# Kernel tuning notes

Measured on AMD Instinct MI355X. Metric: run time of the kernel, lower is better.

## Reference

```python
import jax, jax.numpy as jnp
import numpy as np

VOCAB, EMB, HID = 32000, 512, 1024
B, T = 16, 128


def setup_inputs() -> dict:
    key = jax.random.key(0)
    ks = jax.random.split(key, 12)
    bound = 1.0 / np.sqrt(HID)
    u = lambda k, shape: jax.random.uniform(k, shape, jnp.float32, -bound, bound)
    return {
        "sentence": jax.random.randint(ks[0], (B, T), 0, VOCAB),
        "emb": jax.random.normal(ks[1], (VOCAB, EMB), jnp.float32),
        "W_i": u(ks[2], (EMB + HID, HID)), "b_i": u(ks[3], (HID,)),
        "W_f": u(ks[4], (EMB + HID, HID)), "b_f": u(ks[5], (HID,)),
        "W_o": u(ks[6], (EMB + HID, HID)), "b_o": u(ks[7], (HID,)),
        "W_c": u(ks[8], (EMB + HID, HID)), "b_c": u(ks[9], (HID,)),
        "W_hq": u(ks[10], (HID, VOCAB)), "b_q": u(ks[11], (VOCAB,)),
    }


def reference(sentence, emb, W_i, b_i, W_f, b_f, W_o, b_o, W_c, b_c, W_hq, b_q):
    # [B,T,E] -> [T,B,E]
    x = jnp.swapaxes(emb[sentence], 0, 1)
    # Fuse the 4 gate matmuls into one concatenated-weight matmul (same math).
    W = jnp.concatenate([W_i, W_f, W_o, W_c], axis=1)  # [E+H, 4H]
    b = jnp.concatenate([b_i, b_f, b_o, b_c])          # [4H]
    h0 = jnp.zeros((x.shape[1], HID), x.dtype)

    def step(carry, xt):
        h, c = carry
        z = jnp.concatenate([xt, h], axis=1) @ W + b   # [B,4H]
        i, f, o, g = jnp.split(z, 4, axis=1)
        i, f, o = jax.nn.sigmoid(i), jax.nn.sigmoid(f), jax.nn.sigmoid(o)
        c = f * c + i * jnp.tanh(g)
        h = o * jnp.tanh(c)
        return (h, c), h

    _, hs = jax.lax.scan(step, (h0, h0), x)            # [T,B,H]
    out = jnp.einsum('tbh,hv->tbv', hs, W_hq) + b_q    # [T,B,V]
    return jnp.transpose(out, (1, 2, 0))               # [B,V,T] as in torch permute(1,2,0)
```

## Files before the change

kernel.cpp:

```cpp
#include <hip/hip_runtime.h>
#include <math.h>

typedef float f32x4 __attribute__((ext_vector_type(4)));
typedef short bf16x8 __attribute__((ext_vector_type(8)));
typedef unsigned short u16;
typedef unsigned int u32;
typedef unsigned long long u64;

#define FLAG_STRIDE 16
#define ACQ_BASE    8192
#define EPOCH_BASE  8448
#define QCNT_BASE   8512
#define TCNT_BASE   8528
#define FLAG_WORDS  ((TCNT_BASE + 1) * FLAG_STRIDE)
#define NTILE       125

__device__ __forceinline__ u16 f2bf(float f) {
    union { float f; unsigned u; } x; x.f = f;
    unsigned r = x.u + 0x7fff + ((x.u >> 16) & 1);
    return (u16)(r >> 16);
}

__device__ __forceinline__ void gload_lds16(const u16* g, u16* l) {
    __builtin_amdgcn_global_load_lds(
        (const __attribute__((address_space(1))) void*)g,
        (__attribute__((address_space(3))) void*)l, 16, 0, 0);
}

__global__ __launch_bounds__(256) void prep(
    const int* __restrict__ sent, const float* __restrict__ emb, u16* __restrict__ xb) {
    const int bx = blockIdx.x, tid = threadIdx.x;
    int row = bx * 2 + (tid >> 7);
    int t = row >> 4, b = row & 15;
    int idx = sent[b * 128 + t];
    float4 v = ((const float4*)(emb + (size_t)idx * 512))[tid & 127];
    ushort4 s = { f2bf(v.x), f2bf(v.y), f2bf(v.z), f2bf(v.w) };
    ((ushort4*)(xb + (size_t)row * 512))[tid & 127] = s;
}

__global__ __launch_bounds__(512, 2) void lstm_proj(
    u16* __restrict__ hs,
    const u16* __restrict__ xb,
    const float* __restrict__ Wi, const float* __restrict__ Wf,
    const float* __restrict__ Wo, const float* __restrict__ Wc,
    const float* __restrict__ bi, const float* __restrict__ bf_,
    const float* __restrict__ bo, const float* __restrict__ bc,
    u32* __restrict__ flags,
    const float* __restrict__ Whq,
    u16* __restrict__ whqt,
    const float* __restrict__ bq, float* __restrict__ out) {
    __shared__ __align__(16) char smem[135680];
    const int bx = blockIdx.x;
    const int tid = threadIdx.x;
    const int w = tid >> 6, l = tid & 63;

    if (tid == 0)
        __hip_atomic_fetch_add(&flags[(size_t)(ACQ_BASE + (bx & 255)) * FLAG_STRIDE], 0u,
                               __ATOMIC_ACQ_REL, __HIP_MEMORY_SCOPE_AGENT);

    if (bx < 64) {
        u16* hstage = (u16*)smem;
        u16* xstage = (u16*)(smem + 32768);
        u16* wfx    = (u16*)(smem + 65536);
        float (*zlds)[16][17] = (float (*)[16][17])(void*)(smem + 131072);
        u32* lds_cnt = (u32*)(smem + 135424);
        const int j = bx;
        const int row = l & 15, hi = l >> 4;
        if (tid == 0) *lds_cnt = 0;

        bf16x8 wf[32];
        if (w < 4) {
            const float* Wg = (w == 0) ? Wi : (w == 1) ? Wf : (w == 2) ? Wo : Wc;
#pragma unroll
            for (int kk = 0; kk < 32; ++kk)
#pragma unroll
                for (int e = 0; e < 8; ++e)
                    wf[kk][e] = f2bf(Wg[(size_t)(512 + kk * 32 + hi * 8 + e) * 1024 + j * 16 + row]);
#pragma unroll
            for (int kk = 0; kk < 16; ++kk) {
                bf16x8 v;
#pragma unroll
                for (int e = 0; e < 8; ++e)
                    v[e] = f2bf(Wg[(size_t)(kk * 32 + hi * 8 + e) * 1024 + j * 16 + row]);
                *(bf16x8*)(wfx + ((size_t)(w * 16 + kk) * 64 + l) * 8) = v;
            }
        }
        float bzi = 0.f, bzf = 0.f, bzo = 0.f, bzc = 0.f;
        const int b = tid >> 4, hc = tid & 15;
        if (tid < 256) {
            bzi = bi[j * 16 + hc]; bzf = bf_[j * 16 + hc];
            bzo = bo[j * 16 + hc]; bzc = bc[j * 16 + hc];
        }
#pragma unroll
        for (int q = 0; q < 2; ++q) {
            int jx0 = (w * 2 + q) * 2;
            gload_lds16(xb + (size_t)((l & 31) >> 1) * 512 + (jx0 + (l >> 5)) * 16 + (l & 1) * 8,
                        xstage + (size_t)jx0 * 256);
        }
        __syncthreads();

        float cst = 0.f;

        for (int t = 0; t < 128; ++t) {
            if (t < 127) {
                const u16* xbase = xb + (size_t)(t + 1) * 16 * 512;
                u16* xd = xstage + ((t + 1) & 1) * 8192;
#pragma unroll
                for (int q = 0; q < 2; ++q) {
                    int jx0 = (w * 2 + q) * 2;
                    gload_lds16(xbase + (size_t)((l & 31) >> 1) * 512 + (jx0 + (l >> 5)) * 16 + (l & 1) * 8,
                                xd + (size_t)jx0 * 256);
                }
            }
            if (t > 0) {
                const u16* hbase = hs + (size_t)(t - 1) * 16 * 1024;
                {
                    int spins = 0;
                    while (true) {
                        u32 f = 1u;
                        if (l < 8)
                            f = __hip_atomic_load(
                                    &flags[(size_t)((t - 1) * 64 + 8 * w + l) * FLAG_STRIDE],
                                    __ATOMIC_RELAXED, __HIP_MEMORY_SCOPE_SYSTEM);
                        if (__ballot(f != 0u) == ~0ull) break;
                        __builtin_amdgcn_s_sleep(1);
                        if (++spins > (1 << 20)) break;
                    }
                }
#pragma unroll
                for (int q = 0; q < 4; ++q) {
                    int jw0 = 8 * w + 2 * q;
                    gload_lds16(hbase + (size_t)((l & 31) >> 1) * 1024
                                      + (jw0 + (l >> 5)) * 16 + (l & 1) * 8,
                                hstage + (size_t)jw0 * 256);
                }
            }
            __syncthreads();
            {
                if (t > 0 && tid == 0)
                    __hip_atomic_store(&flags[(size_t)(EPOCH_BASE + j) * FLAG_STRIDE], (u32)t,
                                       __ATOMIC_RELAXED, __HIP_MEMORY_SCOPE_SYSTEM);
                if (w < 4) {
                    const u16* xs = xstage + (t & 1) * 8192;
                    f32x4 zv = { 0.f, 0.f, 0.f, 0.f };
                    f32x4 ac0 = zv, ac1 = zv, ac2 = zv, ac3 = zv;
#pragma unroll
                    for (int kk = 0; kk < 16; kk += 4) {
#pragma unroll
                        for (int u = 0; u < 4; ++u) {
                            int c = kk + u;
                            bf16x8 a = *(const bf16x8*)(xs + (2 * c + (hi >> 1)) * 256
                                                        + row * 16 + (hi & 1) * 8);
                            bf16x8 bx = *(const bf16x8*)(wfx + ((size_t)(w * 16 + c) * 64 + l) * 8);
                            f32x4& ac = (u == 0) ? ac0 : (u == 1) ? ac1 : (u == 2) ? ac2 : ac3;
                            ac = __builtin_amdgcn_mfma_f32_16x16x32_bf16(a, bx, ac, 0, 0, 0);
                        }
                    }
                    if (t > 0) {
#pragma unroll
                        for (int kk = 0; kk < 32; kk += 4) {
#pragma unroll
                            for (int u = 0; u < 4; ++u) {
                                int c = kk + u;
                                int base = (2 * c + (hi >> 1)) * 256 + row * 16 + (hi & 1) * 8;
                                bf16x8 a = *(const bf16x8*)(hstage + base);
                                f32x4& ac = (u == 0) ? ac0 : (u == 1) ? ac1 : (u == 2) ? ac2 : ac3;
                                ac = __builtin_amdgcn_mfma_f32_16x16x32_bf16(a, wf[c], ac, 0, 0, 0);
                            }
                        }
                    }
                    f32x4 acc = (ac0 + ac1) + (ac2 + ac3);
#pragma unroll
                    for (int r = 0; r < 4; ++r)
                        zlds[w][hi * 4 + r][row] = acc[r];
                }
            }
            __syncthreads();
            if (tid < 256) {
                float zi = zlds[0][b][hc] + bzi;
                float zf = zlds[1][b][hc] + bzf;
                float zo = zlds[2][b][hc] + bzo;
                float zc = zlds[3][b][hc] + bzc;
                float ig = 1.f / (1.f + __expf(-zi));
                float fg = 1.f / (1.f + __expf(-zf));
                float og = 1.f / (1.f + __expf(-zo));
                float gg = tanhf(zc);
                cst = fg * cst + ig * gg;
                float h = og * tanhf(cst);
                float hn = __shfl_xor(h, 1);
                if (!(l & 1)) {
                    unsigned pk = (unsigned)f2bf(h) | ((unsigned)f2bf(hn) << 16);
                    u32* dst = (u32*)hs + (((size_t)(t * 16 + b) * 1024 + j * 16 + hc) >> 1);
                    __hip_atomic_store(dst, pk, __ATOMIC_RELAXED, __HIP_MEMORY_SCOPE_SYSTEM);
                }
            }
            if (w < 4) {
                asm volatile("s_waitcnt vmcnt(0)" ::: "memory");
                if (l == 0) {
                    u32 old = atomicAdd(lds_cnt, 1u);
                    if (old == (u32)(4 * t + 3))
                        __hip_atomic_store(&flags[(size_t)(t * 64 + j) * FLAG_STRIDE], 1u,
                                           __ATOMIC_RELAXED, __HIP_MEMORY_SCOPE_SYSTEM);
                }
            }
        }
        if (w == 0) {
            int spins = 0;
            while (true) {
                u32 f = __hip_atomic_load(&flags[(size_t)(127 * 64 + l) * FLAG_STRIDE],
                                          __ATOMIC_RELAXED, __HIP_MEMORY_SCOPE_SYSTEM);
                if (__ballot(f != 0) == ~0ull) break;
                __builtin_amdgcn_s_sleep(1);
                if (++spins > (1 << 20)) break;
            }
            if (l == 0)
                __hip_atomic_store(&flags[(size_t)(EPOCH_BASE + j) * FLAG_STRIDE], 128u,
                                   __ATOMIC_RELAXED, __HIP_MEMORY_SCOPE_SYSTEM);
        }
        return;
    }

    {
        float (*tp)[32][33] = (float (*)[32][33])(void*)smem;
        const int half = tid >> 8, t256 = tid & 255;
        const int r = t256 >> 3, cq = (t256 & 7) * 4;
        const int c = t256 >> 3, rq = (t256 & 7) * 4;
        for (int it = 0; it < 84; ++it) {
            int q = it * 384 + (bx - 64) * 2 + half;
            bool act = q < 32000;
            int rt = 0, ct = 0;
            if (act) { rt = (q / 1000) * 32; ct = (q % 1000) * 32; }
            if (act) {
                float4 v = *(const float4*)(Whq + (size_t)(rt + r) * 32000 + ct + cq);
                tp[half][r][cq] = v.x; tp[half][r][cq + 1] = v.y;
                tp[half][r][cq + 2] = v.z; tp[half][r][cq + 3] = v.w;
            }
            __syncthreads();
            if (act) {
                u64 pk = (u64)f2bf(tp[half][rq][c])
                       | ((u64)f2bf(tp[half][rq + 1][c]) << 16)
                       | ((u64)f2bf(tp[half][rq + 2][c]) << 32)
                       | ((u64)f2bf(tp[half][rq + 3][c]) << 48);
                __hip_atomic_store((u64*)(whqt + (size_t)(ct + c) * 1024 + rt + rq), pk,
                                   __ATOMIC_RELAXED, __HIP_MEMORY_SCOPE_SYSTEM);
            }
            __syncthreads();
        }
        asm volatile("s_waitcnt vmcnt(0)" ::: "memory");
        if (tid == 0)
            __hip_atomic_fetch_add(&flags[(size_t)TCNT_BASE * FLAG_STRIDE], 1u,
                                   __ATOMIC_RELAXED, __HIP_MEMORY_SCOPE_SYSTEM);
    }

    u16* As = (u16*)smem;
    u16* Bs = (u16*)(smem + 32768);
    u32* idx_slot = (u32*)(smem + 98304);
    const int wr = w >> 2, wc = w & 3;
    const int lr = l >> 4, lc = l & 15;

    if (tid == 0)
        *idx_slot = __hip_atomic_fetch_add(&flags[(size_t)QCNT_BASE * FLAG_STRIDE],
                                           1u, __ATOMIC_RELAXED, __HIP_MEMORY_SCOPE_AGENT);
    if (w == 0) {
        int spins = 0;
        while (__hip_atomic_load(&flags[(size_t)TCNT_BASE * FLAG_STRIDE],
                                 __ATOMIC_RELAXED, __HIP_MEMORY_SCOPE_SYSTEM) < 192u) {
            __builtin_amdgcn_s_sleep(8);
            if (++spins > (1 << 20)) break;
        }
    }
    __syncthreads();
    const u32 myIdx = *idx_slot;
    if (myIdx >= NTILE) return;
    const int n0 = (int)myIdx * 256;

    for (int m = 0; m < 16; ++m) {
        if (w == 0) {
            const u32 need = (u32)(8 * m + 8);
            int spins = 0;
            while (__hip_atomic_load(&flags[(size_t)(EPOCH_BASE + (bx & 63)) * FLAG_STRIDE],
                                     __ATOMIC_RELAXED, __HIP_MEMORY_SCOPE_SYSTEM) < need) {
                __builtin_amdgcn_s_sleep(8);
                if (++spins > (1 << 20)) break;
            }
        }
        __syncthreads();

        auto STAGE = [&](int bi, int kt) {
#pragma unroll
            for (int i = 0; i < 2; ++i) {
                int C = i * 512 + tid, r = C >> 3, c = C & 7;
                int sc = c ^ (r & 7);
                int arow = (8 * m + (r & 7)) * 16 + (r >> 3);
                gload_lds16(hs + (size_t)arow * 1024 + kt * 64 + sc * 8,
                            As + (size_t)(bi * 8192 + (i * 512 + w * 64) * 8));
            }
#pragma unroll
            for (int i = 0; i < 4; ++i) {
                int C = i * 512 + tid, r = C >> 3, c = C & 7;
                int sc = c ^ (r & 7);
                gload_lds16(whqt + (size_t)(n0 + r) * 1024 + kt * 64 + sc * 8,
                            Bs + (size_t)(bi * 16384 + (i * 512 + w * 64) * 8));
            }
        };

        f32x4 acc[4][4];
        f32x4 zz = { 0.f, 0.f, 0.f, 0.f };
#pragma unroll
        for (int i = 0; i < 4; i++)
#pragma unroll
            for (int jj = 0; jj < 4; jj++) acc[i][jj] = zz;

        int cur = 0;
        STAGE(0, 0);
        __syncthreads();
        for (int kt = 0; kt < 16; ++kt) {
            if (kt + 1 < 16) STAGE(cur ^ 1, kt + 1);
            const u16* Ab = As + cur * 8192;
            const u16* Bb = Bs + cur * 16384;
#pragma unroll
            for (int kk = 0; kk < 2; ++kk) {
                bf16x8 af[4], bf[4];
#pragma unroll
                for (int mi = 0; mi < 4; ++mi) {
                    int rA = wr * 64 + mi * 16 + lc;
                    int s = (kk * 4 + lr) ^ (rA & 7);
                    af[mi] = *(const bf16x8*)(Ab + rA * 64 + s * 8);
                }
#pragma unroll
                for (int ni = 0; ni < 4; ++ni) {
                    int rB = wc * 64 + ni * 16 + lc;
                    int s = (kk * 4 + lr) ^ (rB & 7);
                    bf[ni] = *(const bf16x8*)(Bb + rB * 64 + s * 8);
                }
#pragma unroll
                for (int mi = 0; mi < 4; ++mi)
#pragma unroll
                    for (int ni = 0; ni < 4; ++ni)
                        acc[mi][ni] = __builtin_amdgcn_mfma_f32_16x16x32_bf16(af[mi], bf[ni], acc[mi][ni], 0, 0, 0);
            }
            __syncthreads();
            cur ^= 1;
        }
#pragma unroll
        for (int ni = 0; ni < 4; ni++) {
            int col = n0 + wc * 64 + ni * 16 + lc;
            float bv = bq[col];
#pragma unroll
            for (int mi = 0; mi < 4; mi++) {
                int r0 = wr * 64 + mi * 16 + lr * 4;
                int bb = r0 >> 3;
                int t0 = 8 * m + (r0 & 7);
                float4 st = { acc[mi][ni][0] + bv, acc[mi][ni][1] + bv,
                              acc[mi][ni][2] + bv, acc[mi][ni][3] + bv };
                *(float4*)(out + (size_t)bb * 4096000 + (size_t)col * 128 + t0) = st;
            }
        }
    }
}

extern "C" void kernel_launch(void* const* d_in, const int* in_sizes, int n_in,
                              void* d_out, int out_size, void* d_ws, size_t ws_size,
                              hipStream_t stream) {
    const int*   sent = (const int*)d_in[0];
    const float* emb  = (const float*)d_in[1];
    const float* W_i  = (const float*)d_in[2];
    const float* b_i  = (const float*)d_in[3];
    const float* W_f  = (const float*)d_in[4];
    const float* b_f  = (const float*)d_in[5];
    const float* W_o  = (const float*)d_in[6];
    const float* b_o  = (const float*)d_in[7];
    const float* W_c  = (const float*)d_in[8];
    const float* b_c  = (const float*)d_in[9];
    const float* W_hq = (const float*)d_in[10];
    const float* b_q  = (const float*)d_in[11];
    float* out = (float*)d_out;

    char* ws = (char*)d_ws;
    size_t off = 0;
    auto alloc = [&](size_t bytes) { void* p = ws + off; off += (bytes + 255) & ~255ull; return p; };
    u32*   flags = (u32*)alloc((size_t)FLAG_WORDS * 4);
    u16*   xb   = (u16*)alloc((size_t)2048 * 512 * 2);
    u16*   hs   = (u16*)alloc((size_t)2048 * 1024 * 2);
    u16*   whqt = (u16*)alloc((size_t)32000 * 1024 * 2);

    hipMemsetAsync(flags, 0, (size_t)FLAG_WORDS * 4, stream);
    prep<<<1024, 256, 0, stream>>>(sent, emb, xb);
    lstm_proj<<<256, 512, 0, stream>>>(hs, xb, W_i, W_f, W_o, W_c,
                                       b_i, b_f, b_o, b_c,
                                       flags, W_hq, whqt, b_q, out);
}
```

Measured before the change: 649.0 us.

## Specialize waves: loaders fetch x/h while compute waves precompute next x-projection

Warps 4-7 now act as dedicated loaders: they prefetch x two steps ahead and do the flag spin-wait plus the h-state staging. Warps 0-3 compute the input projection for step t+1 while waiting, and keep it in registers so only the recurrent h matmul sits on the critical path after the barrier. This aims to shorten the serial per-timestep latency of the recurrence. It adds register pressure for the carried accumulators and relies on the double-buffered xstage indexing being correct.

```diff
diff --git a/kernel.cpp b/kernel.cpp
--- a/kernel.cpp
+++ b/kernel.cpp
@@ -84,6 +84,19 @@
                     v[e] = f2bf(Wg[(size_t)(kk * 32 + hi * 8 + e) * 1024 + j * 16 + row]);
                 *(bf16x8*)(wfx + ((size_t)(w * 16 + kk) * 64 + l) * 8) = v;
             }
+        } else {
+#pragma unroll
+            for (int q = 0; q < 4; ++q) {
+                int jx0 = ((w - 4) * 4 + q) * 2;
+                gload_lds16(xb + (size_t)((l & 31) >> 1) * 512 + (jx0 + (l >> 5)) * 16 + (l & 1) * 8,
+                            xstage + (size_t)jx0 * 256);
+            }
+#pragma unroll
+            for (int q = 0; q < 4; ++q) {
+                int jx0 = ((w - 4) * 4 + q) * 2;
+                gload_lds16(xb + (size_t)(16 * 512 + ((l & 31) >> 1) * 512) + (jx0 + (l >> 5)) * 16 + (l & 1) * 8,
+                            xstage + (size_t)(8192 + jx0 * 256));
+            }
         }
         float bzi = 0.f, bzf = 0.f, bzo = 0.f, bzc = 0.f;
         const int b = tid >> 4, hc = tid & 15;
@@ -91,59 +104,65 @@
             bzi = bi[j * 16 + hc]; bzf = bf_[j * 16 + hc];
             bzo = bo[j * 16 + hc]; bzc = bc[j * 16 + hc];
         }
-#pragma unroll
-        for (int q = 0; q < 2; ++q) {
-            int jx0 = (w * 2 + q) * 2;
-            gload_lds16(xb + (size_t)((l & 31) >> 1) * 512 + (jx0 + (l >> 5)) * 16 + (l & 1) * 8,
-                        xstage + (size_t)jx0 * 256);
-        }
         __syncthreads();
 
+        f32x4 zz4 = { 0.f, 0.f, 0.f, 0.f };
+        f32x4 zxc0 = zz4, zxc1 = zz4, zxc2 = zz4, zxc3 = zz4;
+        if (w < 4) {
+#pragma unroll
+            for (int kk = 0; kk < 16; kk += 4) {
+#pragma unroll
+                for (int u = 0; u < 4; ++u) {
+                    int c = kk + u;
+                    bf16x8 a = *(const bf16x8*)(xstage + (2 * c + (hi >> 1)) * 256
+                                                + row * 16 + (hi & 1) * 8);
+                    bf16x8 bxv = *(const bf16x8*)(wfx + ((size_t)(w * 16 + c) * 64 + l) * 8);
+                    f32x4& ac = (u == 0) ? zxc0 : (u == 1) ? zxc1 : (u == 2) ? zxc2 : zxc3;
+                    ac = __builtin_amdgcn_mfma_f32_16x16x32_bf16(a, bxv, ac, 0, 0, 0);
+                }
+            }
+        }
         float cst = 0.f;
 
         for (int t = 0; t < 128; ++t) {
-            if (t < 127) {
-                const u16* xbase = xb + (size_t)(t + 1) * 16 * 512;
-                u16* xd = xstage + ((t + 1) & 1) * 8192;
-#pragma unroll
-                for (int q = 0; q < 2; ++q) {
-                    int jx0 = (w * 2 + q) * 2;
-                    gload_lds16(xbase + (size_t)((l & 31) >> 1) * 512 + (jx0 + (l >> 5)) * 16 + (l & 1) * 8,
-                                xd + (size_t)jx0 * 256);
-                }
-            }
-            if (t > 0) {
-                const u16* hbase = hs + (size_t)(t - 1) * 16 * 1024;
-                {
-                    int spins = 0;
-                    while (true) {
-                        u32 f = 1u;
-                        if (l < 8)
-                            f = __hip_atomic_load(
-                                    &flags[(size_t)((t - 1) * 64 + 8 * w + l) * FLAG_STRIDE],
-                                    __ATOMIC_RELAXED, __HIP_MEMORY_SCOPE_SYSTEM);
-                        if (__ballot(f != 0u) == ~0ull) break;
-                        __builtin_amdgcn_s_sleep(1);
-                        if (++spins > (1 << 20)) break;
+            f32x4 zxn0 = zz4, zxn1 = zz4, zxn2 = zz4, zxn3 = zz4;
+            if (w >= 4) {
+                if (t < 126) {
+                    const u16* xbase = xb + (size_t)(t + 2) * 16 * 512;
+                    u16* xd = xstage + (t & 1) * 8192;
+#pragma unroll
+                    for (int q = 0; q < 4; ++q) {
+                        int jx0 = ((w - 4) * 4 + q) * 2;
+                        gload_lds16(xbase + (size_t)((l & 31) >> 1) * 512 + (jx0 + (l >> 5)) * 16 + (l & 1) * 8,
+                                    xd + (size_t)jx0 * 256);
                     }
                 }
-#pragma unroll
-                for (int q = 0; q < 4; ++q) {
-                    int jw0 = 8 * w + 2 * q;
-                    gload_lds16(hbase + (size_t)((l & 31) >> 1) * 1024
-                                      + (jw0 + (l >> 5)) * 16 + (l & 1) * 8,
-                                hstage + (size_t)jw0 * 256);
-                }
-            }
-            __syncthreads();
-            {
-                if (t > 0 && tid == 0)
-                    __hip_atomic_store(&flags[(size_t)(EPOCH_BASE + j) * FLAG_STRIDE], (u32)t,
-                                       __ATOMIC_RELAXED, __HIP_MEMORY_SCOPE_SYSTEM);
-                if (w < 4) {
-                    const u16* xs = xstage + (t & 1) * 8192;
-                    f32x4 zv = { 0.f, 0.f, 0.f, 0.f };
-                    f32x4 ac0 = zv, ac1 = zv, ac2 = zv, ac3 = zv;
+                if (t > 0) {
+                    {
+                        int spins = 0;
+                        while (true) {
+                            u32 f = 1u;
+                            if (l < 16)
+                                f = __hip_atomic_load(
+                                        &flags[(size_t)((t - 1) * 64 + (w - 4) * 16 + l) * FLAG_STRIDE],
+                                        __ATOMIC_RELAXED, __HIP_MEMORY_SCOPE_SYSTEM);
+                            if (__ballot(f != 0u) == ~0ull) break;
+                            __builtin_amdgcn_s_sleep(1);
+                            if (++spins > (1 << 20)) break;
+                        }
+                    }
+                    const u16* hbase = hs + (size_t)(t - 1) * 16 * 1024;
+#pragma unroll
+                    for (int q = 0; q < 8; ++q) {
+                        int jw0 = (w - 4) * 16 + 2 * q;
+                        gload_lds16(hbase + (size_t)((l & 31) >> 1) * 1024
+                                          + (jw0 + (l >> 5)) * 16 + (l & 1) * 8,
+                                    hstage + (size_t)jw0 * 256);
+                    }
+                }
+            } else {
+                if (t < 127) {
+                    const u16* xs = xstage + ((t + 1) & 1) * 8192;
 #pragma unroll
                     for (int kk = 0; kk < 16; kk += 4) {
 #pragma unroll
@@ -151,29 +170,36 @@
                             int c = kk + u;
                             bf16x8 a = *(const bf16x8*)(xs + (2 * c + (hi >> 1)) * 256
                                                         + row * 16 + (hi & 1) * 8);
-                            bf16x8 bx = *(const bf16x8*)(wfx + ((size_t)(w * 16 + c) * 64 + l) * 8);
-                            f32x4& ac = (u == 0) ? ac0 : (u == 1) ? ac1 : (u == 2) ? ac2 : ac3;
-                            ac = __builtin_amdgcn_mfma_f32_16x16x32_bf16(a, bx, ac, 0, 0, 0);
+                            bf16x8 bxv = *(const bf16x8*)(wfx + ((size_t)(w * 16 + c) * 64 + l) * 8);
+                            f32x4& ac = (u == 0) ? zxn0 : (u == 1) ? zxn1 : (u == 2) ? zxn2 : zxn3;
+                            ac = __builtin_amdgcn_mfma_f32_16x16x32_bf16(a, bxv, ac, 0, 0, 0);
                         }
                     }
-                    if (t > 0) {
-#pragma unroll
-                        for (int kk = 0; kk < 32; kk += 4) {
-#pragma unroll
-                            for (int u = 0; u < 4; ++u) {
-                                int c = kk + u;
-                                int base = (2 * c + (hi >> 1)) * 256 + row * 16 + (hi & 1) * 8;
-                                bf16x8 a = *(const bf16x8*)(hstage + base);
-                                f32x4& ac = (u == 0) ? ac0 : (u == 1) ? ac1 : (u == 2) ? ac2 : ac3;
-                                ac = __builtin_amdgcn_mfma_f32_16x16x32_bf16(a, wf[c], ac, 0, 0, 0);
-                            }
+                }
+            }
+            __syncthreads();
+            if (t > 0 && tid == 0)
+                __hip_atomic_store(&flags[(size_t)(EPOCH_BASE + j) * FLAG_STRIDE], (u32)t,
+                                   __ATOMIC_RELAXED, __HIP_MEMORY_SCOPE_SYSTEM);
+            if (w < 4) {
+                f32x4 ac0 = zxc0, ac1 = zxc1, ac2 = zxc2, ac3 = zxc3;
+                if (t > 0) {
+#pragma unroll
+                    for (int kk = 0; kk < 32; kk += 4) {
+#pragma unroll
+                        for (int u = 0; u < 4; ++u) {
+                            int c = kk + u;
+                            int base = (2 * c + (hi >> 1)) * 256 + row * 16 + (hi & 1) * 8;
+                            bf16x8 a = *(const bf16x8*)(hstage + base);
+                            f32x4& ac = (u == 0) ? ac0 : (u == 1) ? ac1 : (u == 2) ? ac2 : ac3;
+                            ac = __builtin_amdgcn_mfma_f32_16x16x32_bf16(a, wf[c], ac, 0, 0, 0);
                         }
                     }
-                    f32x4 acc = (ac0 + ac1) + (ac2 + ac3);
-#pragma unroll
-                    for (int r = 0; r < 4; ++r)
-                        zlds[w][hi * 4 + r][row] = acc[r];
-                }
+                }
+                f32x4 acc = (ac0 + ac1) + (ac2 + ac3);
+#pragma unroll
+                for (int r = 0; r < 4; ++r)
+                    zlds[w][hi * 4 + r][row] = acc[r];
             }
             __syncthreads();
             if (tid < 256) {
@@ -202,6 +228,7 @@
                         __hip_atomic_store(&flags[(size_t)(t * 64 + j) * FLAG_STRIDE], 1u,
                                            __ATOMIC_RELAXED, __HIP_MEMORY_SCOPE_SYSTEM);
                 }
+                zxc0 = zxn0; zxc1 = zxn1; zxc2 = zxn2; zxc3 = zxn3;
             }
         }
         if (w == 0) {
```

Result: faster. 628.9 us (median of 2 runs) (-3.1%).
